# Optimization experiments

Hardware: AMD Instinct MI355X
Metric: run time of the kernel (lower is better)

Reference implementation:

```python
import jax, jax.numpy as jnp
import numpy as np
from functools import reduce
from jax.scipy.linalg import expm

C = jnp.complex64
N1 = 5          # qubits
L = 4           # layers
DIM = 2 ** N1   # 32


def _constants():
    # Single-qubit operators (numpy, build-time constants)
    s = np.array([[0, 1], [1, 0]], np.complex64)      # pauli X / 's'
    p = np.eye(2, dtype=np.complex64)                 # identity
    n = np.array([[0, 0], [0, 1]], np.complex64)      # number op
    z = np.array([[1, 0], [0, -1]], np.complex64)     # pauli Z
    kron_chain = lambda ops: reduce(np.kron, ops)

    jc = [1.0, 1.0, 1.0, 1.0]
    omega = -20.0
    rabif = [0.0, 0.0, 0.0, 0.0, omega]
    detun = [2 * jc[0], 2 * jc[1], 2 * jc[2], 2 * jc[3], 2 * sum(jc)]
    inter = [4 * jc[k] for k in range(4)]

    M = np.zeros((DIM, DIM), np.complex64)
    for jq in range(N1):  # rabi drive terms
        M += rabif[jq] * kron_chain([s if i == jq else p for i in range(N1)])
    for jq in range(N1):  # detuning terms (subtracted: matrix - matrix2)
        M -= detun[jq] * kron_chain([n if i == jq else p for i in range(N1)])
    for jq in range(N1 - 1):  # interaction n_j n_{N1-1}
        ops = [n if i == jq else p for i in range(N1 - 1)] + [n]
        M += inter[jq] * kron_chain(ops)

    Zs = np.stack([kron_chain([z if i == q else p for i in range(N1)]) for q in range(N1)])
    Xs = np.stack([kron_chain([s if i == q else p for i in range(N1)]) for q in range(N1)])
    return jnp.asarray(M), jnp.asarray(Zs), jnp.asarray(Xs)

M_CONST, Z_CONST, X_CONST = _constants()
I32 = jnp.eye(DIM, dtype=C)
TIMES = jnp.asarray(np.arange(0.1, 1.0, 0.1), jnp.float32)  # 9 time steps


def _get_U(a, b, g):
    # Product over qubits of (Rz-like)(Rx-like)(Rz-like) rotations, as in source.
    U = I32
    for i in range(N1):
        u1 = jnp.cos(a[i]) * I32 - 1j * jnp.sin(a[i]) * Z_CONST[i]
        u2 = jnp.cos(b[i]) * I32 - 1j * jnp.sin(b[i]) * X_CONST[i]
        u3 = jnp.cos(g[i]) * I32 - 1j * jnp.sin(g[i]) * Z_CONST[i]
        U = u3 @ u2 @ u1 @ U
    return U


def _forward(state, params, W, bias):
    a, b, g = params[0], params[1], params[2]
    # H(t) = expm(-1j * t * M), batched over the 9 time points
    Hs = expm((-1j) * TIMES[:, None, None].astype(C) * M_CONST)  # (9,32,32)
    # torch.kron(state.reshape(4,4), [1,0]).flatten() == kron(state.flatten(), [1,0])
    psi = jnp.kron(state.astype(C), jnp.array([1.0, 0.0], dtype=C))  # (32,)
    s = jnp.broadcast_to(psi, (TIMES.shape[0], DIM))  # (9,32), one state per time
    for l in range(L):
        U1 = _get_U(a[l, 0], b[l, 0], g[l, 0])
        U2 = _get_U(a[l, 1], b[l, 1], g[l, 1])
        s = jnp.einsum('ij,tj->ti', U1, s)
        s = jnp.einsum('tij,tj->ti', Hs, s)
        s = jnp.einsum('ij,tj->ti', U2, s)
    probs = jnp.abs(s) ** 2  # (9,32)
    r = jnp.sum(probs[:, 0::2], axis=1) - jnp.sum(probs[:, 1::2], axis=1)  # (9,)
    r = r.astype(jnp.float32).reshape(1, -1)  # (1,9)
    return jnp.tanh(r @ W.T + bias)  # (1, output_size)


def setup_inputs() -> dict:
    key = jax.random.key(0)
    k1, k2, k3, k4 = jax.random.split(key, 4)
    state = jax.random.normal(k1, (16,), dtype=jnp.float32)
    params = jax.random.normal(k2, (3, L, 2, N1), dtype=jnp.float32)
    W = jax.random.normal(k3, (2, 9), dtype=jnp.float32) * 0.1
    bias = jax.random.normal(k4, (2,), dtype=jnp.float32) * 0.1
    return {"state": state, "params": params, "W": W, "bias": bias}


def reference(state, params, W, bias):
    return _forward(state, params, W, bias)
```

## Files before the change

kernel.cpp:

```cpp
#include <hip/hip_runtime.h>
#include <math.h>


struct C2 { float x, y; };
__device__ __forceinline__ C2 cmul(C2 a, C2 b){ return {a.x*b.x - a.y*b.y, a.x*b.y + a.y*b.x}; }
__device__ __forceinline__ C2 cadd(C2 a, C2 b){ return {a.x+b.x, a.y+b.y}; }

template<int MASK>
__device__ __forceinline__ float xl(float v){
    int i = __builtin_bit_cast(int, v), r;
    if constexpr (MASK == 1)      r = __builtin_amdgcn_mov_dpp(i, 0xB1, 0xF, 0xF, true);
    else if constexpr (MASK == 2) r = __builtin_amdgcn_mov_dpp(i, 0x4E, 0xF, 0xF, true);
    else                          r = __builtin_amdgcn_ds_swizzle(i, (MASK << 10) | 0x1F);
    return __builtin_bit_cast(float, r);
}
template<int MASK>
__device__ __forceinline__ C2 xl2(C2 v){ return { xl<MASK>(v.x), xl<MASK>(v.y) }; }

template<int MASK>
__device__ __forceinline__ C2 pair_op(C2 amp, C2 dg, C2 of){
    C2 p = xl2<MASK>(amp);
    return cadd(cmul(dg, amp), cmul(of, p));
}

__device__ __forceinline__ void gate_coeffs(float a, float b, float g, bool hi, C2& dg, C2& of){
    float spg, cpg, samg, camg, sb, cb;
    __sincosf(a + g, &spg, &cpg);
    __sincosf(a - g, &samg, &camg);
    __sincosf(b,     &sb,  &cb);
    dg = { cb * cpg, hi ?  cb * spg : -cb * spg };
    of = { hi ? -sb * samg : sb * samg, -sb * camg };
}

template<int I>
__device__ __forceinline__ void gate(const float* __restrict__ params, int base, int lane32, C2& amp){
    constexpr int MASK = 1 << (4 - I);
    const float a = params[base + I], b = params[40 + base + I], g = params[80 + base + I];
    C2 dg, of;
    gate_coeffs(a, b, g, (lane32 & MASK) != 0, dg, of);
    amp = pair_op<MASK>(amp, dg, of);
}

__global__ __launch_bounds__(320)
void qp_kernel(const float* __restrict__ state,
               const float* __restrict__ params,
               const float* __restrict__ W,
               const float* __restrict__ bias,
               float* __restrict__ out)
{
    __shared__ float r_lds[9];

    const int tid    = threadIdx.x;
    const int lane32 = tid & 31;
    const int tstep  = tid >> 5;
    const float t    = 0.1f * (float)(tstep + 1);

    C2 amp = { (lane32 & 1) ? 0.f : state[lane32 >> 1], 0.f };

    const int  b0  = lane32 & 1;
    const float fm = (float)__popc(lane32 >> 1);
    const float hds = (b0 ? 1.f : -1.f) * (2.f * fm - 4.f);
    const float Om  = sqrtf(hds * hds + 400.f);
    float sth, cth; __sincosf(Om * t, &sth, &cth);
    const float k = sth / Om;
    float s4, c4;  __sincosf(4.f * t, &s4, &c4);
    const C2 ph = { c4, s4 };
    const C2 hdg = cmul(ph, C2{ cth, -k * hds });
    const C2 hof = cmul(ph, C2{ 0.f, 20.f * k });

    #pragma unroll
    for (int l = 0; l < 4; ++l) {
        const int bA = l * 10, bB = l * 10 + 5;
        gate<0>(params, bA, lane32, amp);
        gate<1>(params, bA, lane32, amp);
        gate<2>(params, bA, lane32, amp);
        gate<3>(params, bA, lane32, amp);
        {
            const float a = params[bA + 4], b = params[40 + bA + 4], g = params[80 + bA + 4];
            C2 dg, of; gate_coeffs(a, b, g, b0 != 0, dg, of);
            const C2 ndg = cadd(cmul(hdg, dg), cmul(hof, C2{ -of.x,  of.y }));
            const C2 nof = cadd(cmul(hdg, of), cmul(hof, C2{  dg.x, -dg.y }));
            amp = pair_op<1>(amp, ndg, nof);
        }
        gate<0>(params, bB, lane32, amp);
        gate<1>(params, bB, lane32, amp);
        gate<2>(params, bB, lane32, amp);
        gate<3>(params, bB, lane32, amp);
        gate<4>(params, bB, lane32, amp);
    }

    const float p = amp.x * amp.x + amp.y * amp.y;
    float sp = b0 ? -p : p;
    sp += xl<16>(sp);
    sp += xl<8>(sp);
    sp += xl<4>(sp);
    sp += xl<2>(sp);
    sp += xl<1>(sp);
    if (lane32 == 0 && tstep < 9) r_lds[tstep] = sp;
    __syncthreads();

    if (tid < 2) {
        float acc = bias[tid];
        #pragma unroll
        for (int q = 0; q < 9; ++q) acc += r_lds[q] * W[tid * 9 + q];
        out[tid] = tanhf(acc);
    }
}

extern "C" void kernel_launch(void* const* d_in, const int* in_sizes, int n_in,
                              void* d_out, int out_size, void* d_ws, size_t ws_size,
                              hipStream_t stream) {
    const float* state  = (const float*)d_in[0];
    const float* params = (const float*)d_in[1];
    const float* W      = (const float*)d_in[2];
    const float* bias   = (const float*)d_in[3];
    float* out = (float*)d_out;
    qp_kernel<<<1, 320, 0, stream>>>(state, params, W, bias, out);
}
```

Baseline: 11.72 us.

## Fuse single-qubit gate pairs into two-qubit updates and prefetch output weights

Pairs of adjacent single-qubit gates are combined into one two-qubit update per lane. It reads three shuffled neighbours (A, B, A^B) and applies precomputed product coefficients, which shortens the serial chain of cross-lane exchanges. W and bias loads are moved to the kernel start so their latency overlaps the main compute. Sincos calls are split into separate __sinf/__cosf. The trade is more complex multiplies per step and extra swizzles for the combined mask.

```diff
diff --git a/kernel.cpp b/kernel.cpp
--- a/kernel.cpp
+++ b/kernel.cpp
@@ -11,6 +11,7 @@
     int i = __builtin_bit_cast(int, v), r;
     if constexpr (MASK == 1)      r = __builtin_amdgcn_mov_dpp(i, 0xB1, 0xF, 0xF, true);
     else if constexpr (MASK == 2) r = __builtin_amdgcn_mov_dpp(i, 0x4E, 0xF, 0xF, true);
+    else if constexpr (MASK == 3) r = __builtin_amdgcn_mov_dpp(i, 0x1B, 0xF, 0xF, true);
     else                          r = __builtin_amdgcn_ds_swizzle(i, (MASK << 10) | 0x1F);
     return __builtin_bit_cast(float, r);
 }
@@ -23,22 +24,27 @@
     return cadd(cmul(dg, amp), cmul(of, p));
 }
 
-__device__ __forceinline__ void gate_coeffs(float a, float b, float g, bool hi, C2& dg, C2& of){
-    float spg, cpg, samg, camg, sb, cb;
-    __sincosf(a + g, &spg, &cpg);
-    __sincosf(a - g, &samg, &camg);
-    __sincosf(b,     &sb,  &cb);
+template<int MA, int MB>
+__device__ __forceinline__ C2 pair2(C2 amp, C2 dgA, C2 ofA, C2 dgB, C2 ofB){
+    const C2 aB  = xl2<MB>(amp);
+    const C2 aA  = xl2<MA>(amp);
+    const C2 aAB = xl2<MA ^ MB>(amp);
+    const C2 c00 = cmul(dgA, dgB);
+    const C2 c0B = cmul(dgA, ofB);
+    const C2 cA0 = cmul(ofA, dgB);
+    const C2 cAB = cmul(ofA, ofB);
+    return cadd(cadd(cmul(c00, amp), cmul(c0B, aB)),
+                cadd(cmul(cA0, aA), cmul(cAB, aAB)));
+}
+
+__device__ __forceinline__ void gc(const float* __restrict__ params, int idx, bool hi,
+                                   C2& dg, C2& of){
+    const float a = params[idx], b = params[40 + idx], g = params[80 + idx];
+    const float spg = __sinf(a + g), cpg = __cosf(a + g);
+    const float samg = __sinf(a - g), camg = __cosf(a - g);
+    const float sb = __sinf(b), cb = __cosf(b);
     dg = { cb * cpg, hi ?  cb * spg : -cb * spg };
     of = { hi ? -sb * samg : sb * samg, -sb * camg };
-}
-
-template<int I>
-__device__ __forceinline__ void gate(const float* __restrict__ params, int base, int lane32, C2& amp){
-    constexpr int MASK = 1 << (4 - I);
-    const float a = params[base + I], b = params[40 + base + I], g = params[80 + base + I];
-    C2 dg, of;
-    gate_coeffs(a, b, g, (lane32 & MASK) != 0, dg, of);
-    amp = pair_op<MASK>(amp, dg, of);
 }
 
 __global__ __launch_bounds__(320)
@@ -55,38 +61,63 @@
     const int tstep  = tid >> 5;
     const float t    = 0.1f * (float)(tstep + 1);
 
-    C2 amp = { (lane32 & 1) ? 0.f : state[lane32 >> 1], 0.f };
+    float wreg[9]; float breg = 0.f;
+    if (tid < 2) {
+        breg = bias[tid];
+        #pragma unroll
+        for (int q = 0; q < 9; ++q) wreg[q] = W[tid * 9 + q];
+    }
 
-    const int  b0  = lane32 & 1;
-    const float fm = (float)__popc(lane32 >> 1);
+    const int b0 = lane32 & 1;
+    C2 amp = { b0 ? 0.f : state[lane32 >> 1], 0.f };
+
+    const float fm  = (float)__popc(lane32 >> 1);
     const float hds = (b0 ? 1.f : -1.f) * (2.f * fm - 4.f);
     const float Om  = sqrtf(hds * hds + 400.f);
-    float sth, cth; __sincosf(Om * t, &sth, &cth);
-    const float k = sth / Om;
-    float s4, c4;  __sincosf(4.f * t, &s4, &c4);
-    const C2 ph = { c4, s4 };
+    const float sth = __sinf(Om * t), cth = __cosf(Om * t);
+    const float k   = sth / Om;
+    const float s4  = __sinf(4.f * t), c4 = __cosf(4.f * t);
+    const C2 ph  = { c4, s4 };
     const C2 hdg = cmul(ph, C2{ cth, -k * hds });
     const C2 hof = cmul(ph, C2{ 0.f, 20.f * k });
 
     #pragma unroll
     for (int l = 0; l < 4; ++l) {
-        const int bA = l * 10, bB = l * 10 + 5;
-        gate<0>(params, bA, lane32, amp);
-        gate<1>(params, bA, lane32, amp);
-        gate<2>(params, bA, lane32, amp);
-        gate<3>(params, bA, lane32, amp);
+        const int bA = l * 10, bB = bA + 5;
         {
-            const float a = params[bA + 4], b = params[40 + bA + 4], g = params[80 + bA + 4];
-            C2 dg, of; gate_coeffs(a, b, g, b0 != 0, dg, of);
+            C2 dgA, ofA, dgB, ofB;
+            gc(params, bA + 0, (lane32 & 16) != 0, dgA, ofA);
+            gc(params, bA + 1, (lane32 &  8) != 0, dgB, ofB);
+            amp = pair2<16, 8>(amp, dgA, ofA, dgB, ofB);
+        }
+        {
+            C2 dgA, ofA, dgB, ofB;
+            gc(params, bA + 2, (lane32 & 4) != 0, dgA, ofA);
+            gc(params, bA + 3, (lane32 & 2) != 0, dgB, ofB);
+            amp = pair2<4, 2>(amp, dgA, ofA, dgB, ofB);
+        }
+        {
+            C2 dg, of; gc(params, bA + 4, b0 != 0, dg, of);
             const C2 ndg = cadd(cmul(hdg, dg), cmul(hof, C2{ -of.x,  of.y }));
             const C2 nof = cadd(cmul(hdg, of), cmul(hof, C2{  dg.x, -dg.y }));
             amp = pair_op<1>(amp, ndg, nof);
         }
-        gate<0>(params, bB, lane32, amp);
-        gate<1>(params, bB, lane32, amp);
-        gate<2>(params, bB, lane32, amp);
-        gate<3>(params, bB, lane32, amp);
-        gate<4>(params, bB, lane32, amp);
+        {
+            C2 dgA, ofA, dgB, ofB;
+            gc(params, bB + 0, (lane32 & 16) != 0, dgA, ofA);
+            gc(params, bB + 1, (lane32 &  8) != 0, dgB, ofB);
+            amp = pair2<16, 8>(amp, dgA, ofA, dgB, ofB);
+        }
+        {
+            C2 dgA, ofA, dgB, ofB;
+            gc(params, bB + 2, (lane32 & 4) != 0, dgA, ofA);
+            gc(params, bB + 3, (lane32 & 2) != 0, dgB, ofB);
+            amp = pair2<4, 2>(amp, dgA, ofA, dgB, ofB);
+        }
+        {
+            C2 dg, of; gc(params, bB + 4, b0 != 0, dg, of);
+            amp = pair_op<1>(amp, dg, of);
+        }
     }
 
     const float p = amp.x * amp.x + amp.y * amp.y;
@@ -100,9 +131,9 @@
     __syncthreads();
 
     if (tid < 2) {
-        float acc = bias[tid];
+        float acc = breg;
         #pragma unroll
-        for (int q = 0; q < 9; ++q) acc += r_lds[q] * W[tid * 9 + q];
+        for (int q = 0; q < 9; ++q) acc += r_lds[q] * wreg[q];
         out[tid] = tanhf(acc);
     }
 }
```

Result: slower. 12.61 us (+7.6%).
